# Optimization experiments

Hardware: AMD Instinct MI355X
Metric: run time of the kernel (lower is better)

The kernel has to match this reference:

```python
import jax, jax.numpy as jnp
import numpy as np

ANNEAL = 0.01

def _tsig(x, temp=ANNEAL):
    # temperature sigmoid with +/-50 clipping as in the torch source
    return jax.nn.sigmoid(jnp.clip(x / temp, -50.0, 50.0))

def setup_inputs() -> dict:
    key = jax.random.key(0)
    k1, k2 = jax.random.split(key)
    N, D = 512, 512
    preds = jax.random.normal(k1, (N, D), dtype=jnp.float32)
    labels = jax.random.randint(k2, (N,), 0, 64, dtype=jnp.int64)
    return {"preds": preds, "labels": labels}

def reference(preds, labels):
    N = preds.shape[0]
    dtype = preds.dtype
    eye = jnp.eye(N, dtype=dtype)
    same = (labels[:, None] == labels[None, :]).astype(dtype)
    I_pos = same * (1.0 - eye)                      # positives excl. self
    sim_mat = preds @ preds.T                       # [N, N]
    # sim_diff[i, j, k] = sim_mat[i, k] - sim_mat[i, j]
    sim_sg = _tsig(sim_mat[:, None, :] - sim_mat[:, :, None]) * (1.0 - eye)[None, :, :]
    sim_all_rk = 1.0 + jnp.sum(sim_sg, axis=-1)     # [N, N]
    # sum_k sim_sg[i,j,k] * I_pos[i,k]
    pos_sum = jnp.einsum('ijk,ik->ij', sim_sg, I_pos)
    sim_pos_rk = eye + I_pos + I_pos * pos_sum      # [N, N]
    n_pos = jnp.sum(I_pos, axis=1) + 1.0            # [N]
    per_anchor = jnp.sum(sim_pos_rk / sim_all_rk, axis=1) / n_pos
    per_anchor = jnp.where(n_pos > 1.0, per_anchor, 0.0)  # skip anchors with no positives
    ap = jnp.sum(per_anchor) / N
    return 1.0 - ap
```

## Files before the change

kernel.cpp:

```cpp
#include <hip/hip_runtime.h>
#include <hip/hip_bf16.h>

#define NN 512

__global__ __launch_bounds__(256) void sap_gemm(const float* __restrict__ P,
                                                float* __restrict__ S) {
    __shared__ float As[32][33];
    __shared__ float Bs[32][33];
    const int t  = threadIdx.x;
    const int tx = t & 15, ty = t >> 4;
    const int i0 = blockIdx.y * 32, j0 = blockIdx.x * 32;

    float acc00 = 0.f, acc01 = 0.f, acc10 = 0.f, acc11 = 0.f;

    const int lr = t >> 3;
    const int lc = (t & 7) * 4;

    for (int kt = 0; kt < NN; kt += 32) {
        float4 a = *(const float4*)&P[(i0 + lr) * NN + kt + lc];
        float4 b = *(const float4*)&P[(j0 + lr) * NN + kt + lc];
        As[lr][lc + 0] = a.x; As[lr][lc + 1] = a.y;
        As[lr][lc + 2] = a.z; As[lr][lc + 3] = a.w;
        Bs[lr][lc + 0] = b.x; Bs[lr][lc + 1] = b.y;
        Bs[lr][lc + 2] = b.z; Bs[lr][lc + 3] = b.w;
        __syncthreads();
#pragma unroll
        for (int kk = 0; kk < 32; kk++) {
            float a0 = As[2 * ty][kk],     a1 = As[2 * ty + 1][kk];
            float b0 = Bs[2 * tx][kk],     b1 = Bs[2 * tx + 1][kk];
            acc00 += a0 * b0; acc01 += a0 * b1;
            acc10 += a1 * b0; acc11 += a1 * b1;
        }
        __syncthreads();
    }
    const int i = i0 + 2 * ty, j = j0 + 2 * tx;
    S[i * NN + j]           = acc00;
    S[i * NN + j + 1]       = acc01;
    S[(i + 1) * NN + j]     = acc10;
    S[(i + 1) * NN + j + 1] = acc11;
}

__global__ __launch_bounds__(256) void sap_rows(const float* __restrict__ S,
                                               const int* __restrict__ labels,
                                               float* __restrict__ per_anchor) {
    __shared__ float srow[NN];
    __shared__ float posf[NN];
    __shared__ int   poslist[NN];
    __shared__ int   npos_cnt;
    __shared__ float wave_part[4];

    const int i = blockIdx.x;
    const int t = threadIdx.x;
    if (t == 0) npos_cnt = 0;
    if (t < 4) wave_part[t] = 0.f;
    __syncthreads();

    const int li = labels[i];
    for (int k = t; k < NN; k += 256) {
        srow[k] = S[i * NN + k];
        bool p  = (labels[k] == li) && (k != i);
        posf[k] = p ? 1.f : 0.f;
        if (p) {
            int idx = atomicAdd(&npos_cnt, 1);
            poslist[idx] = k;
        }
    }
    __syncthreads();

    const int cnt = npos_cnt;
    if (cnt == 0) {
        if (t == 0) per_anchor[i] = 0.f;
        return;
    }

    const int wave = t >> 6, lane = t & 63;
    const float C1   = 100.0f * 1.44269504088896340736f;
    const float CLIP = 50.0f * 1.44269504088896340736f;

    float acc = 0.f;
    for (int idx = wave; idx <= cnt; idx += 4) {
        const int   j   = (idx == cnt) ? i : poslist[idx];
        const float sij = srow[j];
        float sum_all = 0.f, sum_pos = 0.f;
#pragma unroll
        for (int kk = 0; kk < 8; kk++) {
            const int   k  = lane + (kk << 6);
            float y = (sij - srow[k]) * C1;
            y = fminf(fmaxf(y, -CLIP), CLIP);
            float tt = 1.0f / (1.0f + exp2f(y));
            if (k == j) tt = 0.f;
            sum_all += tt;
            sum_pos += tt * posf[k];
        }
#pragma unroll
        for (int off = 32; off; off >>= 1) {
            sum_all += __shfl_down(sum_all, off);
            sum_pos += __shfl_down(sum_pos, off);
        }
        if (lane == 0) {
            const float den = 1.0f + sum_all;
            const float num = (j == i) ? 1.0f : (1.0f + sum_pos);
            acc += num / den;
        }
    }
    if (lane == 0) wave_part[wave] = acc;
    __syncthreads();
    if (t == 0) {
        float tot = wave_part[0] + wave_part[1] + wave_part[2] + wave_part[3];
        per_anchor[i] = tot / (float)(cnt + 1);
    }
}

__global__ __launch_bounds__(256) void sap_reduce(const float* __restrict__ per_anchor,
                                                  float* __restrict__ out) {
    __shared__ float sh[256];
    const int t = threadIdx.x;
    sh[t] = per_anchor[t] + per_anchor[t + 256];
    __syncthreads();
    for (int s = 128; s; s >>= 1) {
        if (t < s) sh[t] += sh[t + s];
        __syncthreads();
    }
    if (t == 0) out[0] = 1.0f - sh[0] / (float)NN;
}

extern "C" void kernel_launch(void* const* d_in, const int* in_sizes, int n_in,
                              void* d_out, int out_size, void* d_ws, size_t ws_size,
                              hipStream_t stream) {
    const float* preds  = (const float*)d_in[0];
    const int*   labels = (const int*)d_in[1];
    float* out = (float*)d_out;

    float* S          = (float*)d_ws;
    float* per_anchor = (float*)d_ws + NN * NN;

    dim3 ggrid(NN / 32, NN / 32);
    sap_gemm<<<ggrid, 256, 0, stream>>>(preds, S);
    sap_rows<<<NN, 256, 0, stream>>>(S, labels, per_anchor);
    sap_reduce<<<1, 256, 0, stream>>>(per_anchor, out);
}
```

Baseline: 78.99 us.

## Fuse similarity GEMM into per-anchor ranking kernel, two anchors per block

The separate GEMM kernel and the global similarity matrix are removed. Each block now computes the two similarity rows for its pair of anchors straight from preds, with each thread producing dot products against two columns, and keeps the rows in shared memory for the ranking loop. This drops one launch and the round trip of the NxN matrix through global memory. In exchange, each block rereads the whole preds matrix (1 MB) from global or L2 with per-thread row-strided float4 loads. The GEMM work is also spread over only 256 blocks and loses the shared-memory tile reuse it had before.

```diff
diff --git a/kernel.cpp b/kernel.cpp
--- a/kernel.cpp
+++ b/kernel.cpp
@@ -1,113 +1,105 @@
 #include <hip/hip_runtime.h>
-#include <hip/hip_bf16.h>
 
 #define NN 512
 
-__global__ __launch_bounds__(256) void sap_gemm(const float* __restrict__ P,
-                                                float* __restrict__ S) {
-    __shared__ float As[32][33];
-    __shared__ float Bs[32][33];
-    const int t  = threadIdx.x;
-    const int tx = t & 15, ty = t >> 4;
-    const int i0 = blockIdx.y * 32, j0 = blockIdx.x * 32;
-
-    float acc00 = 0.f, acc01 = 0.f, acc10 = 0.f, acc11 = 0.f;
-
-    const int lr = t >> 3;
-    const int lc = (t & 7) * 4;
-
-    for (int kt = 0; kt < NN; kt += 32) {
-        float4 a = *(const float4*)&P[(i0 + lr) * NN + kt + lc];
-        float4 b = *(const float4*)&P[(j0 + lr) * NN + kt + lc];
-        As[lr][lc + 0] = a.x; As[lr][lc + 1] = a.y;
-        As[lr][lc + 2] = a.z; As[lr][lc + 3] = a.w;
-        Bs[lr][lc + 0] = b.x; Bs[lr][lc + 1] = b.y;
-        Bs[lr][lc + 2] = b.z; Bs[lr][lc + 3] = b.w;
-        __syncthreads();
-#pragma unroll
-        for (int kk = 0; kk < 32; kk++) {
-            float a0 = As[2 * ty][kk],     a1 = As[2 * ty + 1][kk];
-            float b0 = Bs[2 * tx][kk],     b1 = Bs[2 * tx + 1][kk];
-            acc00 += a0 * b0; acc01 += a0 * b1;
-            acc10 += a1 * b0; acc11 += a1 * b1;
-        }
-        __syncthreads();
-    }
-    const int i = i0 + 2 * ty, j = j0 + 2 * tx;
-    S[i * NN + j]           = acc00;
-    S[i * NN + j + 1]       = acc01;
-    S[(i + 1) * NN + j]     = acc10;
-    S[(i + 1) * NN + j + 1] = acc11;
-}
-
-__global__ __launch_bounds__(256) void sap_rows(const float* __restrict__ S,
-                                               const int* __restrict__ labels,
-                                               float* __restrict__ per_anchor) {
-    __shared__ float srow[NN];
+__global__ __launch_bounds__(256) void sap_fused(const float* __restrict__ P,
+                                                 const int* __restrict__ labels,
+                                                 float* __restrict__ per_anchor) {
+    __shared__ __align__(16) float arow[2][NN];
+    __shared__ __align__(16) float srow[2][NN];
+    __shared__ __align__(16) int   labels_sh[NN];
     __shared__ float posf[NN];
     __shared__ int   poslist[NN];
     __shared__ int   npos_cnt;
     __shared__ float wave_part[4];
 
-    const int i = blockIdx.x;
-    const int t = threadIdx.x;
-    if (t == 0) npos_cnt = 0;
-    if (t < 4) wave_part[t] = 0.f;
+    const int t  = threadIdx.x;
+    const int i0 = blockIdx.x * 2;
+
+    ((float4*)&arow[0][0])[t] = ((const float4*)&P[i0 * NN])[t];
+    if (t < 128) ((int4*)labels_sh)[t] = ((const int4*)labels)[t];
     __syncthreads();
 
-    const int li = labels[i];
-    for (int k = t; k < NN; k += 256) {
-        srow[k] = S[i * NN + k];
-        bool p  = (labels[k] == li) && (k != i);
-        posf[k] = p ? 1.f : 0.f;
-        if (p) {
-            int idx = atomicAdd(&npos_cnt, 1);
-            poslist[idx] = k;
+    {
+        const float4* B0 = (const float4*)&P[t * NN];
+        const float4* B1 = (const float4*)&P[(t + 256) * NN];
+        const float4* A0 = (const float4*)&arow[0][0];
+        const float4* A1 = (const float4*)&arow[1][0];
+        float s00 = 0.f, s01 = 0.f, s10 = 0.f, s11 = 0.f;
+#pragma unroll 8
+        for (int c = 0; c < NN / 4; ++c) {
+            float4 b0 = B0[c];
+            float4 b1 = B1[c];
+            float4 a0 = A0[c];
+            float4 a1 = A1[c];
+            s00 += a0.x * b0.x; s00 += a0.y * b0.y; s00 += a0.z * b0.z; s00 += a0.w * b0.w;
+            s01 += a1.x * b0.x; s01 += a1.y * b0.y; s01 += a1.z * b0.z; s01 += a1.w * b0.w;
+            s10 += a0.x * b1.x; s10 += a0.y * b1.y; s10 += a0.z * b1.z; s10 += a0.w * b1.w;
+            s11 += a1.x * b1.x; s11 += a1.y * b1.y; s11 += a1.z * b1.z; s11 += a1.w * b1.w;
         }
-    }
-    __syncthreads();
-
-    const int cnt = npos_cnt;
-    if (cnt == 0) {
-        if (t == 0) per_anchor[i] = 0.f;
-        return;
+        srow[0][t]       = s00;
+        srow[1][t]       = s01;
+        srow[0][t + 256] = s10;
+        srow[1][t + 256] = s11;
     }
 
     const int wave = t >> 6, lane = t & 63;
     const float C1   = 100.0f * 1.44269504088896340736f;
-    const float CLIP = 50.0f * 1.44269504088896340736f;
+    const float CLIP = 50.0f  * 1.44269504088896340736f;
 
-    float acc = 0.f;
-    for (int idx = wave; idx <= cnt; idx += 4) {
-        const int   j   = (idx == cnt) ? i : poslist[idx];
-        const float sij = srow[j];
-        float sum_all = 0.f, sum_pos = 0.f;
+    for (int a = 0; a < 2; ++a) {
+        const int i  = i0 + a;
+        const int li = labels_sh[i];
+        __syncthreads();
+        if (t == 0) npos_cnt = 0;
+        if (t < 4) wave_part[t] = 0.f;
+        __syncthreads();
+        for (int k = t; k < NN; k += 256) {
+            bool p  = (labels_sh[k] == li) && (k != i);
+            posf[k] = p ? 1.f : 0.f;
+            if (p) { int idx = atomicAdd(&npos_cnt, 1); poslist[idx] = k; }
+        }
+        __syncthreads();
+
+        const int cnt = npos_cnt;
+        if (cnt == 0) {
+            if (t == 0) per_anchor[i] = 0.f;
+            continue;
+        }
+
+        const float* sr = srow[a];
+        float acc = 0.f;
+        for (int idx = wave; idx <= cnt; idx += 4) {
+            const int   j   = (idx == cnt) ? i : poslist[idx];
+            const float sij = sr[j];
+            float sum_all = 0.f, sum_pos = 0.f;
 #pragma unroll
-        for (int kk = 0; kk < 8; kk++) {
-            const int   k  = lane + (kk << 6);
-            float y = (sij - srow[k]) * C1;
-            y = fminf(fmaxf(y, -CLIP), CLIP);
-            float tt = 1.0f / (1.0f + exp2f(y));
-            if (k == j) tt = 0.f;
-            sum_all += tt;
-            sum_pos += tt * posf[k];
+            for (int kk = 0; kk < 8; kk++) {
+                const int k = lane + (kk << 6);
+                float y = (sij - sr[k]) * C1;
+                y = fminf(fmaxf(y, -CLIP), CLIP);
+                float tt = 1.0f / (1.0f + exp2f(y));
+                if (k == j) tt = 0.f;
+                sum_all += tt;
+                sum_pos += tt * posf[k];
+            }
+#pragma unroll
+            for (int off = 32; off; off >>= 1) {
+                sum_all += __shfl_down(sum_all, off);
+                sum_pos += __shfl_down(sum_pos, off);
+            }
+            if (lane == 0) {
+                const float den = 1.0f + sum_all;
+                const float num = (j == i) ? 1.0f : (1.0f + sum_pos);
+                acc += num / den;
+            }
         }
-#pragma unroll
-        for (int off = 32; off; off >>= 1) {
-            sum_all += __shfl_down(sum_all, off);
-            sum_pos += __shfl_down(sum_pos, off);
+        if (lane == 0) wave_part[wave] = acc;
+        __syncthreads();
+        if (t == 0) {
+            per_anchor[i] = (wave_part[0] + wave_part[1] + wave_part[2] + wave_part[3])
+                          / (float)(cnt + 1);
         }
-        if (lane == 0) {
-            const float den = 1.0f + sum_all;
-            const float num = (j == i) ? 1.0f : (1.0f + sum_pos);
-            acc += num / den;
-        }
-    }
-    if (lane == 0) wave_part[wave] = acc;
-    __syncthreads();
-    if (t == 0) {
-        float tot = wave_part[0] + wave_part[1] + wave_part[2] + wave_part[3];
-        per_anchor[i] = tot / (float)(cnt + 1);
     }
 }
 
@@ -129,13 +121,9 @@
                               hipStream_t stream) {
     const float* preds  = (const float*)d_in[0];
     const int*   labels = (const int*)d_in[1];
-    float* out = (float*)d_out;
+    float* out        = (float*)d_out;
+    float* per_anchor = (float*)d_ws;
 
-    float* S          = (float*)d_ws;
-    float* per_anchor = (float*)d_ws + NN * NN;
-
-    dim3 ggrid(NN / 32, NN / 32);
-    sap_gemm<<<ggrid, 256, 0, stream>>>(preds, S);
-    sap_rows<<<NN, 256, 0, stream>>>(S, labels, per_anchor);
+    sap_fused<<<NN / 2, 256, 0, stream>>>(preds, labels, per_anchor);
     sap_reduce<<<1, 256, 0, stream>>>(per_anchor, out);
 }
```

Result: slower. 94.45 us (+19.6%).

## Fuse GEMM, row pass and reduction into one persistent kernel with flag barriers

Applied to the files above, without the earlier changes.

Merges the three kernel launches into a single 256-block kernel. Each block computes one GEMM tile, then all blocks meet at a global flag barrier, and each block processes two anchor rows. Block 0 waits on a second barrier, resets the flags and does the final reduction. This removes two launch gaps, but it relies on all 256 blocks being co-resident for the spin barrier. It also halves the parallelism of the row phase, and relies on the workspace flags starting at zero on the first call.

```diff
diff --git a/kernel.cpp b/kernel.cpp
--- a/kernel.cpp
+++ b/kernel.cpp
@@ -1,120 +1,141 @@
 #include <hip/hip_runtime.h>
-#include <hip/hip_bf16.h>
 
 #define NN 512
+#define MAGIC1 0x4D379A21u
+#define MAGIC2 0xB6E58C37u
 
-__global__ __launch_bounds__(256) void sap_gemm(const float* __restrict__ P,
-                                                float* __restrict__ S) {
+__device__ __forceinline__ void flag_signal(unsigned* __restrict__ flags, unsigned magic) {
+    __syncthreads();
+    if (threadIdx.x == 0)
+        __hip_atomic_store(&flags[blockIdx.x], magic,
+                           __ATOMIC_RELEASE, __HIP_MEMORY_SCOPE_AGENT);
+}
+__device__ __forceinline__ void flag_wait_all(unsigned* __restrict__ flags, unsigned magic) {
+    while (__hip_atomic_load(&flags[threadIdx.x], magic ? __ATOMIC_ACQUIRE : __ATOMIC_ACQUIRE,
+                             __HIP_MEMORY_SCOPE_AGENT) != magic)
+        __builtin_amdgcn_s_sleep(2);
+    __syncthreads();
+}
+
+__global__ __launch_bounds__(256) void sap_one(const float* __restrict__ P,
+                                               const int* __restrict__ labels,
+                                               float* __restrict__ S,
+                                               float* __restrict__ per_anchor,
+                                               unsigned* __restrict__ flag1,
+                                               unsigned* __restrict__ flag2,
+                                               float* __restrict__ out) {
     __shared__ float As[32][33];
     __shared__ float Bs[32][33];
-    const int t  = threadIdx.x;
-    const int tx = t & 15, ty = t >> 4;
-    const int i0 = blockIdx.y * 32, j0 = blockIdx.x * 32;
-
-    float acc00 = 0.f, acc01 = 0.f, acc10 = 0.f, acc11 = 0.f;
-
-    const int lr = t >> 3;
-    const int lc = (t & 7) * 4;
-
-    for (int kt = 0; kt < NN; kt += 32) {
-        float4 a = *(const float4*)&P[(i0 + lr) * NN + kt + lc];
-        float4 b = *(const float4*)&P[(j0 + lr) * NN + kt + lc];
-        As[lr][lc + 0] = a.x; As[lr][lc + 1] = a.y;
-        As[lr][lc + 2] = a.z; As[lr][lc + 3] = a.w;
-        Bs[lr][lc + 0] = b.x; Bs[lr][lc + 1] = b.y;
-        Bs[lr][lc + 2] = b.z; Bs[lr][lc + 3] = b.w;
-        __syncthreads();
-#pragma unroll
-        for (int kk = 0; kk < 32; kk++) {
-            float a0 = As[2 * ty][kk],     a1 = As[2 * ty + 1][kk];
-            float b0 = Bs[2 * tx][kk],     b1 = Bs[2 * tx + 1][kk];
-            acc00 += a0 * b0; acc01 += a0 * b1;
-            acc10 += a1 * b0; acc11 += a1 * b1;
-        }
-        __syncthreads();
-    }
-    const int i = i0 + 2 * ty, j = j0 + 2 * tx;
-    S[i * NN + j]           = acc00;
-    S[i * NN + j + 1]       = acc01;
-    S[(i + 1) * NN + j]     = acc10;
-    S[(i + 1) * NN + j + 1] = acc11;
-}
-
-__global__ __launch_bounds__(256) void sap_rows(const float* __restrict__ S,
-                                               const int* __restrict__ labels,
-                                               float* __restrict__ per_anchor) {
     __shared__ float srow[NN];
     __shared__ float posf[NN];
     __shared__ int   poslist[NN];
     __shared__ int   npos_cnt;
     __shared__ float wave_part[4];
+    __shared__ float sh[256];
 
-    const int i = blockIdx.x;
     const int t = threadIdx.x;
-    if (t == 0) npos_cnt = 0;
-    if (t < 4) wave_part[t] = 0.f;
-    __syncthreads();
+    const int b = blockIdx.x;
 
-    const int li = labels[i];
-    for (int k = t; k < NN; k += 256) {
-        srow[k] = S[i * NN + k];
-        bool p  = (labels[k] == li) && (k != i);
-        posf[k] = p ? 1.f : 0.f;
-        if (p) {
-            int idx = atomicAdd(&npos_cnt, 1);
-            poslist[idx] = k;
+    {
+        const int tx = t & 15, ty = t >> 4;
+        const int i0 = (b >> 4) * 32, j0 = (b & 15) * 32;
+        float acc00 = 0.f, acc01 = 0.f, acc10 = 0.f, acc11 = 0.f;
+        const int lr = t >> 3;
+        const int lc = (t & 7) * 4;
+
+        for (int kt = 0; kt < NN; kt += 32) {
+            float4 a  = *(const float4*)&P[(i0 + lr) * NN + kt + lc];
+            float4 bb = *(const float4*)&P[(j0 + lr) * NN + kt + lc];
+            As[lr][lc + 0] = a.x;  As[lr][lc + 1] = a.y;
+            As[lr][lc + 2] = a.z;  As[lr][lc + 3] = a.w;
+            Bs[lr][lc + 0] = bb.x; Bs[lr][lc + 1] = bb.y;
+            Bs[lr][lc + 2] = bb.z; Bs[lr][lc + 3] = bb.w;
+            __syncthreads();
+#pragma unroll
+            for (int kk = 0; kk < 32; kk++) {
+                float a0 = As[2 * ty][kk], a1 = As[2 * ty + 1][kk];
+                float b0 = Bs[2 * tx][kk], b1 = Bs[2 * tx + 1][kk];
+                acc00 += a0 * b0; acc01 += a0 * b1;
+                acc10 += a1 * b0; acc11 += a1 * b1;
+            }
+            __syncthreads();
         }
+        const int i = i0 + 2 * ty, j = j0 + 2 * tx;
+        S[i * NN + j]           = acc00;
+        S[i * NN + j + 1]       = acc01;
+        S[(i + 1) * NN + j]     = acc10;
+        S[(i + 1) * NN + j + 1] = acc11;
     }
-    __syncthreads();
 
-    const int cnt = npos_cnt;
-    if (cnt == 0) {
-        if (t == 0) per_anchor[i] = 0.f;
-        return;
-    }
+    flag_signal(flag1, MAGIC1);
+    flag_wait_all(flag1, MAGIC1);
 
     const int wave = t >> 6, lane = t & 63;
     const float C1   = 100.0f * 1.44269504088896340736f;
-    const float CLIP = 50.0f * 1.44269504088896340736f;
+    const float CLIP = 50.0f  * 1.44269504088896340736f;
 
-    float acc = 0.f;
-    for (int idx = wave; idx <= cnt; idx += 4) {
-        const int   j   = (idx == cnt) ? i : poslist[idx];
-        const float sij = srow[j];
-        float sum_all = 0.f, sum_pos = 0.f;
+    for (int a = 0; a < 2; ++a) {
+        const int i = 2 * b + a;
+        __syncthreads();
+        if (t == 0) npos_cnt = 0;
+        if (t < 4) wave_part[t] = 0.f;
+        __syncthreads();
+        const int li = labels[i];
+        for (int k = t; k < NN; k += 256) {
+            srow[k] = S[i * NN + k];
+            bool p  = (labels[k] == li) && (k != i);
+            posf[k] = p ? 1.f : 0.f;
+            if (p) { int idx = atomicAdd(&npos_cnt, 1); poslist[idx] = k; }
+        }
+        __syncthreads();
+
+        const int cnt = npos_cnt;
+        if (cnt == 0) {
+            if (t == 0) per_anchor[i] = 0.f;
+            continue;
+        }
+
+        float acc = 0.f;
+        for (int idx = wave; idx <= cnt; idx += 4) {
+            const int   j   = (idx == cnt) ? i : poslist[idx];
+            const float sij = srow[j];
+            float sum_all = 0.f, sum_pos = 0.f;
 #pragma unroll
-        for (int kk = 0; kk < 8; kk++) {
-            const int   k  = lane + (kk << 6);
-            float y = (sij - srow[k]) * C1;
-            y = fminf(fmaxf(y, -CLIP), CLIP);
-            float tt = 1.0f / (1.0f + exp2f(y));
-            if (k == j) tt = 0.f;
-            sum_all += tt;
-            sum_pos += tt * posf[k];
+            for (int kk = 0; kk < 8; kk++) {
+                const int k = lane + (kk << 6);
+                float y = (sij - srow[k]) * C1;
+                y = fminf(fmaxf(y, -CLIP), CLIP);
+                float tt = 1.0f / (1.0f + exp2f(y));
+                if (k == j) tt = 0.f;
+                sum_all += tt;
+                sum_pos += tt * posf[k];
+            }
+#pragma unroll
+            for (int off = 32; off; off >>= 1) {
+                sum_all += __shfl_down(sum_all, off);
+                sum_pos += __shfl_down(sum_pos, off);
+            }
+            if (lane == 0) {
+                const float den = 1.0f + sum_all;
+                acc += ((j == i) ? 1.0f : (1.0f + sum_pos)) / den;
+            }
         }
-#pragma unroll
-        for (int off = 32; off; off >>= 1) {
-            sum_all += __shfl_down(sum_all, off);
-            sum_pos += __shfl_down(sum_pos, off);
-        }
-        if (lane == 0) {
-            const float den = 1.0f + sum_all;
-            const float num = (j == i) ? 1.0f : (1.0f + sum_pos);
-            acc += num / den;
+        if (lane == 0) wave_part[wave] = acc;
+        __syncthreads();
+        if (t == 0) {
+            per_anchor[i] = (wave_part[0] + wave_part[1] + wave_part[2] + wave_part[3])
+                          / (float)(cnt + 1);
         }
     }
-    if (lane == 0) wave_part[wave] = acc;
-    __syncthreads();
-    if (t == 0) {
-        float tot = wave_part[0] + wave_part[1] + wave_part[2] + wave_part[3];
-        per_anchor[i] = tot / (float)(cnt + 1);
-    }
-}
 
-__global__ __launch_bounds__(256) void sap_reduce(const float* __restrict__ per_anchor,
-                                                  float* __restrict__ out) {
-    __shared__ float sh[256];
-    const int t = threadIdx.x;
+    flag_signal(flag2, MAGIC2);
+    if (b != 0) return;
+
+    flag_wait_all(flag2, MAGIC2);
+
+    __hip_atomic_store(&flag1[t], 0u, __ATOMIC_RELAXED, __HIP_MEMORY_SCOPE_AGENT);
+    __hip_atomic_store(&flag2[t], 0u, __ATOMIC_RELAXED, __HIP_MEMORY_SCOPE_AGENT);
+
     sh[t] = per_anchor[t] + per_anchor[t + 256];
     __syncthreads();
     for (int s = 128; s; s >>= 1) {
@@ -131,11 +152,11 @@
     const int*   labels = (const int*)d_in[1];
     float* out = (float*)d_out;
 
-    float* S          = (float*)d_ws;
-    float* per_anchor = (float*)d_ws + NN * NN;
+    float*    S          = (float*)d_ws;
+    float*    per_anchor = (float*)d_ws + NN * NN;
+    unsigned* flag1      = (unsigned*)((float*)d_ws + NN * NN + NN);
+    unsigned* flag2      = flag1 + 256;
 
-    dim3 ggrid(NN / 32, NN / 32);
-    sap_gemm<<<ggrid, 256, 0, stream>>>(preds, S);
-    sap_rows<<<NN, 256, 0, stream>>>(S, labels, per_anchor);
-    sap_reduce<<<1, 256, 0, stream>>>(per_anchor, out);
+    sap_one<<<NN / 2, 256, 0, stream>>>(preds, labels, S, per_anchor,
+                                        flag1, flag2, out);
 }
```

Result: slower. 109.6 us (+38.7%).

## Fuse final reduction into row kernel via flag-based grid handoff

Applied to the files above, without the earlier changes.

Each row block now processes two anchors instead of one, halving the grid to 256 blocks. Each block publishes its two per-anchor values plus a magic flag to global memory. Block 0 spins on all flags, resets them, and performs the final reduction, which removes the separate reduce kernel launch. This relies on block 0 being resident while the others finish and on relaxed atomics plus s_waitcnt for ordering, so the handoff is fragile and there is a risk of deadlock or stale reads.

```diff
diff --git a/kernel.cpp b/kernel.cpp
--- a/kernel.cpp
+++ b/kernel.cpp
@@ -1,7 +1,7 @@
 #include <hip/hip_runtime.h>
-#include <hip/hip_bf16.h>
 
 #define NN 512
+#define FMAGIC 0x5AD0F1A6u
 
 __global__ __launch_bounds__(256) void sap_gemm(const float* __restrict__ P,
                                                 float* __restrict__ S) {
@@ -40,82 +40,107 @@
     S[(i + 1) * NN + j + 1] = acc11;
 }
 
-__global__ __launch_bounds__(256) void sap_rows(const float* __restrict__ S,
-                                               const int* __restrict__ labels,
-                                               float* __restrict__ per_anchor) {
+__global__ __launch_bounds__(256) void sap_rows2(const float* __restrict__ S,
+                                                 const int* __restrict__ labels,
+                                                 unsigned* __restrict__ pa_bits,
+                                                 unsigned* __restrict__ flags,
+                                                 float* __restrict__ out) {
     __shared__ float srow[NN];
     __shared__ float posf[NN];
     __shared__ int   poslist[NN];
     __shared__ int   npos_cnt;
     __shared__ float wave_part[4];
+    __shared__ float pa_out[2];
+    __shared__ float sh[256];
 
-    const int i = blockIdx.x;
     const int t = threadIdx.x;
-    if (t == 0) npos_cnt = 0;
-    if (t < 4) wave_part[t] = 0.f;
-    __syncthreads();
+    const int b = blockIdx.x;
+    const int i0 = 2 * b;
+    const int wave = t >> 6, lane = t & 63;
+    const float C1   = 100.0f * 1.44269504088896340736f;
+    const float CLIP = 50.0f  * 1.44269504088896340736f;
 
-    const int li = labels[i];
-    for (int k = t; k < NN; k += 256) {
-        srow[k] = S[i * NN + k];
-        bool p  = (labels[k] == li) && (k != i);
-        posf[k] = p ? 1.f : 0.f;
-        if (p) {
-            int idx = atomicAdd(&npos_cnt, 1);
-            poslist[idx] = k;
+    for (int a = 0; a < 2; ++a) {
+        const int i = i0 + a;
+        __syncthreads();
+        if (t == 0) npos_cnt = 0;
+        if (t < 4) wave_part[t] = 0.f;
+        __syncthreads();
+        const int li = labels[i];
+        for (int k = t; k < NN; k += 256) {
+            srow[k] = S[i * NN + k];
+            bool p  = (labels[k] == li) && (k != i);
+            posf[k] = p ? 1.f : 0.f;
+            if (p) { int idx = atomicAdd(&npos_cnt, 1); poslist[idx] = k; }
+        }
+        __syncthreads();
+
+        const int cnt = npos_cnt;
+        if (cnt == 0) {
+            if (t == 0) pa_out[a] = 0.f;
+            continue;
+        }
+
+        float acc = 0.f;
+        for (int idx = wave; idx <= cnt; idx += 4) {
+            const int   j   = (idx == cnt) ? i : poslist[idx];
+            const float sij = srow[j];
+            float sum_all = 0.f, sum_pos = 0.f;
+#pragma unroll
+            for (int kk = 0; kk < 8; kk++) {
+                const int k = lane + (kk << 6);
+                float y = (sij - srow[k]) * C1;
+                y = fminf(fmaxf(y, -CLIP), CLIP);
+                float tt = 1.0f / (1.0f + exp2f(y));
+                if (k == j) tt = 0.f;
+                sum_all += tt;
+                sum_pos += tt * posf[k];
+            }
+#pragma unroll
+            for (int off = 32; off; off >>= 1) {
+                sum_all += __shfl_down(sum_all, off);
+                sum_pos += __shfl_down(sum_pos, off);
+            }
+            if (lane == 0) {
+                const float den = 1.0f + sum_all;
+                acc += ((j == i) ? 1.0f : (1.0f + sum_pos)) / den;
+            }
+        }
+        if (lane == 0) wave_part[wave] = acc;
+        __syncthreads();
+        if (t == 0) {
+            pa_out[a] = (wave_part[0] + wave_part[1] + wave_part[2] + wave_part[3])
+                      / (float)(cnt + 1);
         }
     }
     __syncthreads();
 
-    const int cnt = npos_cnt;
-    if (cnt == 0) {
-        if (t == 0) per_anchor[i] = 0.f;
-        return;
+    if (t == 0) {
+        __hip_atomic_store(&pa_bits[i0],     __float_as_uint(pa_out[0]),
+                           __ATOMIC_RELAXED, __HIP_MEMORY_SCOPE_AGENT);
+        __hip_atomic_store(&pa_bits[i0 + 1], __float_as_uint(pa_out[1]),
+                           __ATOMIC_RELAXED, __HIP_MEMORY_SCOPE_AGENT);
+        asm volatile("s_waitcnt vmcnt(0)" ::: "memory");
+        __hip_atomic_store(&flags[b], FMAGIC,
+                           __ATOMIC_RELAXED, __HIP_MEMORY_SCOPE_AGENT);
     }
 
-    const int wave = t >> 6, lane = t & 63;
-    const float C1   = 100.0f * 1.44269504088896340736f;
-    const float CLIP = 50.0f * 1.44269504088896340736f;
+    if (b != 0) return;
 
-    float acc = 0.f;
-    for (int idx = wave; idx <= cnt; idx += 4) {
-        const int   j   = (idx == cnt) ? i : poslist[idx];
-        const float sij = srow[j];
-        float sum_all = 0.f, sum_pos = 0.f;
-#pragma unroll
-        for (int kk = 0; kk < 8; kk++) {
-            const int   k  = lane + (kk << 6);
-            float y = (sij - srow[k]) * C1;
-            y = fminf(fmaxf(y, -CLIP), CLIP);
-            float tt = 1.0f / (1.0f + exp2f(y));
-            if (k == j) tt = 0.f;
-            sum_all += tt;
-            sum_pos += tt * posf[k];
-        }
-#pragma unroll
-        for (int off = 32; off; off >>= 1) {
-            sum_all += __shfl_down(sum_all, off);
-            sum_pos += __shfl_down(sum_pos, off);
-        }
-        if (lane == 0) {
-            const float den = 1.0f + sum_all;
-            const float num = (j == i) ? 1.0f : (1.0f + sum_pos);
-            acc += num / den;
-        }
+    while (__hip_atomic_load(&flags[t], __ATOMIC_RELAXED,
+                             __HIP_MEMORY_SCOPE_AGENT) != FMAGIC)
+        __builtin_amdgcn_s_sleep(8);
+    __hip_atomic_store(&flags[t], 0u, __ATOMIC_RELAXED,
+                       __HIP_MEMORY_SCOPE_AGENT);
+    __syncthreads();
+
+    {
+        float v0 = __uint_as_float(__hip_atomic_load(&pa_bits[t], __ATOMIC_RELAXED,
+                                                     __HIP_MEMORY_SCOPE_AGENT));
+        float v1 = __uint_as_float(__hip_atomic_load(&pa_bits[t + 256], __ATOMIC_RELAXED,
+                                                     __HIP_MEMORY_SCOPE_AGENT));
+        sh[t] = v0 + v1;
     }
-    if (lane == 0) wave_part[wave] = acc;
-    __syncthreads();
-    if (t == 0) {
-        float tot = wave_part[0] + wave_part[1] + wave_part[2] + wave_part[3];
-        per_anchor[i] = tot / (float)(cnt + 1);
-    }
-}
-
-__global__ __launch_bounds__(256) void sap_reduce(const float* __restrict__ per_anchor,
-                                                  float* __restrict__ out) {
-    __shared__ float sh[256];
-    const int t = threadIdx.x;
-    sh[t] = per_anchor[t] + per_anchor[t + 256];
     __syncthreads();
     for (int s = 128; s; s >>= 1) {
         if (t < s) sh[t] += sh[t + s];
@@ -131,11 +156,11 @@
     const int*   labels = (const int*)d_in[1];
     float* out = (float*)d_out;
 
-    float* S          = (float*)d_ws;
-    float* per_anchor = (float*)d_ws + NN * NN;
+    float*    S       = (float*)d_ws;
+    unsigned* pa_bits = (unsigned*)((float*)d_ws + NN * NN);
+    unsigned* flags   = pa_bits + NN;
 
     dim3 ggrid(NN / 32, NN / 32);
     sap_gemm<<<ggrid, 256, 0, stream>>>(preds, S);
-    sap_rows<<<NN, 256, 0, stream>>>(S, labels, per_anchor);
-    sap_reduce<<<1, 256, 0, stream>>>(per_anchor, out);
+    sap_rows2<<<NN / 2, 256, 0, stream>>>(S, labels, pa_bits, flags, out);
 }
```

New measurement: 82.29 us. 1.04x slower.
